# Optimization experiments

Hardware: AMD Instinct MI355X
Metric: run time of the kernel (lower is better)

The kernel has to match this reference:

```python
import jax, jax.numpy as jnp
import numpy as np

N_ATOMS, N_EDGES, N_TRIPLES = 5000, 200000, 4000000
D_NODE, D_EDGE, N_BASIS = 128, 128, 9


def setup_inputs() -> dict:
    key = jax.random.key(0)
    ks = jax.random.split(key, 14)
    inp = {
        "node_feat": jax.random.normal(ks[0], (N_ATOMS, D_NODE), jnp.float32),
        "edge_feat": jax.random.normal(ks[1], (N_EDGES, D_EDGE), jnp.float32),
        "three_basis": jax.random.normal(ks[2], (N_TRIPLES, N_BASIS), jnp.float32),
        "three_cutoff": jax.random.uniform(ks[3], (N_EDGES,), jnp.float32),
        # learned params: update_network_atom = Linear(d_node->n_basis) + sigmoid
        "W_atom": jax.random.normal(ks[4], (D_NODE, N_BASIS), jnp.float32) / np.sqrt(D_NODE).astype(np.float32),
        "b_atom": jnp.zeros((N_BASIS,), jnp.float32),
        # update_network_bond = gated MLP: silu(Linear) * sigmoid(Linear), n_basis->d_edge
        "W_gate": jax.random.normal(ks[5], (N_BASIS, D_EDGE), jnp.float32) / np.sqrt(N_BASIS).astype(np.float32),
        "b_gate": jnp.zeros((D_EDGE,), jnp.float32),
        "W_sig": jax.random.normal(ks[6], (N_BASIS, D_EDGE), jnp.float32) / np.sqrt(N_BASIS).astype(np.float32),
        "b_sig": jnp.zeros((D_EDGE,), jnp.float32),
        # graph structure (int constants)
        "graph_dst": jax.random.randint(ks[7], (N_EDGES,), 0, N_ATOMS, jnp.int32),
        "lg_src": jax.random.randint(ks[8], (N_TRIPLES,), 0, N_EDGES, jnp.int32),
        "lg_dst": jax.random.randint(ks[9], (N_TRIPLES,), 0, N_EDGES, jnp.int32),
        # sorted segment ids == get_segment_indices_from_n(n_triple_ij)
        "segment_ids": jnp.sort(jax.random.randint(ks[10], (N_TRIPLES,), 0, N_EDGES, jnp.int32)),
    }
    return inp


def reference(node_feat, edge_feat, three_basis, three_cutoff,
              W_atom, b_atom, W_gate, b_gate, W_sig, b_sig,
              graph_dst, lg_src, lg_dst, segment_ids):
    # Eq.2: transform node features, gather end atom of each triple's second bond
    atoms = jax.nn.sigmoid(node_feat @ W_atom + b_atom)          # [n_atoms, n_basis]
    end_atom_index = graph_dst[lg_dst]                           # [n_triples]
    basis = three_basis * atoms[end_atom_index]                  # [n_triples, n_basis]
    # cutoff weights per triple (dead code in the provided source: scatter uses basis)
    weights = three_cutoff[lg_src] * three_cutoff[lg_dst]        # [n_triples]
    _ = basis * weights[:, None]
    # scatter-sum triples back to their bond
    new_bonds = jax.ops.segment_sum(basis, segment_ids, num_segments=N_EDGES)  # [n_edges, n_basis]
    # Eq.3: gated MLP bond update
    update = jax.nn.silu(new_bonds @ W_gate + b_gate) * jax.nn.sigmoid(new_bonds @ W_sig + b_sig)
    return edge_feat + update
```

## Files before the change

kernel.cpp:

```cpp
#include <hip/hip_runtime.h>

#define D_NODE    128
#define N_BASIS   9
#define AH_STRIDE 16
#define D_EDGE    128

#define BLOCK_C 512
#define TPT     2
#define CHUNK   (BLOCK_C * TPT)
#define SEG_CAP 384

typedef _Float16 half8 __attribute__((ext_vector_type(8)));

#define AS1(p) ((const __attribute__((address_space(1))) void*)(p))
#define AS3(p) ((__attribute__((address_space(3))) void*)(p))

__device__ __forceinline__ float fast_sigmoid(float x) {
    return __builtin_amdgcn_rcpf(1.0f + __expf(-x));
}

__global__ __launch_bounds__(256) void atoms_kernel(
    const float* __restrict__ node_feat,
    const float* __restrict__ W_atom,
    const float* __restrict__ b_atom,
    _Float16* __restrict__ atoms, int n_atoms)
{
    __shared__ float sW[D_NODE * N_BASIS];
    for (int t = threadIdx.x; t < D_NODE * N_BASIS; t += 256)
        sW[t] = W_atom[t];
    __syncthreads();
    int idx = blockIdx.x * 256 + threadIdx.x;
    int total = n_atoms * N_BASIS;
    if (idx >= total) return;
    int a = idx / N_BASIS;
    int b = idx - a * N_BASIS;
    const float* row = node_feat + a * D_NODE;
    float acc = b_atom[b];
#pragma unroll 8
    for (int i = 0; i < D_NODE; ++i)
        acc += row[i] * sW[i * N_BASIS + b];
    atoms[a * AH_STRIDE + b] = (_Float16)fast_sigmoid(acc);
}

#define FLUSH_RUN()                                                          \
    do {                                                                     \
        if (use_lds) {                                                       \
            float* dst_ = lacc + (cur - seg_first) * N_BASIS;                \
            _Pragma("unroll")                                                \
            for (int k_ = 0; k_ < N_BASIS; ++k_)                             \
                atomicAdd(&dst_[k_], sum[k_]);                               \
        } else {                                                             \
            float* dst_ = new_bonds + (size_t)cur * N_BASIS;                 \
            _Pragma("unroll")                                                \
            for (int k_ = 0; k_ < N_BASIS; ++k_)                             \
                unsafeAtomicAdd(&dst_[k_], sum[k_]);                         \
        }                                                                    \
    } while (0)

__global__ __launch_bounds__(BLOCK_C) void triple_kernel(
    const float* __restrict__ three_basis,
    const _Float16* __restrict__ atoms,
    const int*   __restrict__ graph_dst,
    const int*   __restrict__ lg_dst,
    const int*   __restrict__ seg,
    float* __restrict__ new_bonds,
    int n_triples)
{
    __shared__ float stb[CHUNK * N_BASIS];
    __shared__ float lacc[SEG_CAP * N_BASIS];
    __shared__ int sh_first, sh_last;

    const int tid = threadIdx.x;
    const int chunk_start = blockIdx.x * CHUNK;
    const int t0 = chunk_start + tid * TPT;

    {
        int avail = (n_triples - chunk_start) * (N_BASIS * 4);
        int full_bytes = avail > CHUNK * N_BASIS * 4 ? CHUNK * N_BASIS * 4 : avail;
        int nfull = full_bytes >> 4;
        const char* gsrc = (const char*)three_basis + (size_t)chunk_start * (N_BASIS * 4);
        const int lane = tid & 63;
        for (int base = (tid >> 6) * 64; base < nfull; base += BLOCK_C) {
            int i = base + lane;
            if (i < nfull) {
                __builtin_amdgcn_global_load_lds(
                    AS1(gsrc + (size_t)i * 16),
                    AS3((char*)stb + (size_t)base * 16),
                    16, 0, 0);
            }
        }
        int rem = full_bytes - (nfull << 4);
        if ((tid << 2) < rem)
            ((float*)stb)[nfull * 4 + tid] = ((const float*)gsrc)[nfull * 4 + tid];
    }

    if (tid == 0) sh_first = seg[chunk_start];
    if (tid == BLOCK_C - 1) {
        int last = chunk_start + CHUNK;
        if (last > n_triples) last = n_triples;
        sh_last = seg[last - 1];
    }
    for (int i = tid; i < SEG_CAP * N_BASIS; i += BLOCK_C)
        lacc[i] = 0.0f;

    const bool fast = (t0 + TPT <= n_triples);
    int sg0 = 0, sg1 = 0;
    half8 h0, h1;
    _Float16 e0h = (_Float16)0.f, e1h = (_Float16)0.f;
    if (fast) {
        int2 sg2 = *(const int2*)(seg + t0);
        int2 ld2 = *(const int2*)(lg_dst + t0);
        sg0 = sg2.x; sg1 = sg2.y;
        int ai0 = graph_dst[ld2.x];
        int ai1 = graph_dst[ld2.y];
        const _Float16* ap0 = atoms + (size_t)ai0 * AH_STRIDE;
        const _Float16* ap1 = atoms + (size_t)ai1 * AH_STRIDE;
        h0 = *(const half8*)ap0;
        h1 = *(const half8*)ap1;
        e0h = ap0[8];
        e1h = ap1[8];
    }

    __syncthreads();

    const int seg_first = sh_first;
    const int range = sh_last - seg_first + 1;
    const bool use_lds = (range <= SEG_CAP);

    if (fast) {
        const float* tbl = stb + tid * (TPT * N_BASIS);
        float sum[N_BASIS];
        int cur = sg0;
#pragma unroll
        for (int k = 0; k < 8; ++k) sum[k] = tbl[k] * (float)h0[k];
        sum[8] = tbl[8] * (float)e0h;
        if (sg1 != cur) {
            FLUSH_RUN();
            cur = sg1;
#pragma unroll
            for (int k = 0; k < 8; ++k) sum[k] = tbl[N_BASIS + k] * (float)h1[k];
            sum[8] = tbl[N_BASIS + 8] * (float)e1h;
        } else {
#pragma unroll
            for (int k = 0; k < 8; ++k) sum[k] += tbl[N_BASIS + k] * (float)h1[k];
            sum[8] += tbl[N_BASIS + 8] * (float)e1h;
        }
        FLUSH_RUN();
    } else if (t0 < n_triples) {
        int tend = t0 + TPT; if (tend > n_triples) tend = n_triples;
        for (int t = t0; t < tend; ++t) {
            int cur = seg[t];
            int atom = graph_dst[lg_dst[t]];
            const float* tbr = three_basis + (size_t)t * N_BASIS;
            const _Float16* ar = atoms + (size_t)atom * AH_STRIDE;
            float sum[N_BASIS];
#pragma unroll
            for (int k = 0; k < N_BASIS; ++k) sum[k] = tbr[k] * (float)ar[k];
            FLUSH_RUN();
        }
    }

    __syncthreads();

    if (use_lds) {
        int total = range * N_BASIS;
        for (int idx = tid; idx < total; idx += BLOCK_C) {
            int r = idx / N_BASIS;
            int k = idx - r * N_BASIS;
            float v = lacc[idx];
            int s = seg_first + r;
            if (r == 0 || r == range - 1) {
                if (v != 0.0f)
                    unsafeAtomicAdd(&new_bonds[(size_t)s * N_BASIS + k], v);
            } else {
                new_bonds[(size_t)s * N_BASIS + k] = v;
            }
        }
    }
}

__global__ __launch_bounds__(256) void mlp_kernel(
    const float* __restrict__ edge_feat,
    const float* __restrict__ new_bonds,
    const float* __restrict__ W_gate, const float* __restrict__ b_gate,
    const float* __restrict__ W_sig,  const float* __restrict__ b_sig,
    float* __restrict__ out, int n_edges)
{
    const int tid  = threadIdx.x;
    const int grp  = tid >> 5;
    const int c    = (tid & 31) * 4;
    const int e0   = (blockIdx.x * 8 + grp) * 4;
    if (e0 >= n_edges) return;
    const int nvalid = (n_edges - e0) < 4 ? (n_edges - e0) : 4;

    float nb[4][N_BASIS];
#pragma unroll
    for (int j = 0; j < 4; ++j) {
        const float* nbr = new_bonds + (size_t)(e0 + (j < nvalid ? j : 0)) * N_BASIS;
#pragma unroll
        for (int k = 0; k < N_BASIS; ++k) nb[j][k] = nbr[k];
    }

    float4 bg = *(const float4*)(b_gate + c);
    float4 bs = *(const float4*)(b_sig + c);
    float4 g[4], s[4];
#pragma unroll
    for (int j = 0; j < 4; ++j) { g[j] = bg; s[j] = bs; }

#pragma unroll
    for (int k = 0; k < N_BASIS; ++k) {
        float4 wg = *(const float4*)(W_gate + k * D_EDGE + c);
        float4 ws = *(const float4*)(W_sig  + k * D_EDGE + c);
#pragma unroll
        for (int j = 0; j < 4; ++j) {
            g[j].x += nb[j][k] * wg.x; g[j].y += nb[j][k] * wg.y;
            g[j].z += nb[j][k] * wg.z; g[j].w += nb[j][k] * wg.w;
            s[j].x += nb[j][k] * ws.x; s[j].y += nb[j][k] * ws.y;
            s[j].z += nb[j][k] * ws.z; s[j].w += nb[j][k] * ws.w;
        }
    }

#pragma unroll
    for (int j = 0; j < 4; ++j) {
        if (j < nvalid) {
            int e = e0 + j;
            float4 ef = *(const float4*)(edge_feat + (size_t)e * D_EDGE + c);
            float4 o;
            o.x = ef.x + g[j].x * fast_sigmoid(g[j].x) * fast_sigmoid(s[j].x);
            o.y = ef.y + g[j].y * fast_sigmoid(g[j].y) * fast_sigmoid(s[j].y);
            o.z = ef.z + g[j].z * fast_sigmoid(g[j].z) * fast_sigmoid(s[j].z);
            o.w = ef.w + g[j].w * fast_sigmoid(g[j].w) * fast_sigmoid(s[j].w);
            *(float4*)(out + (size_t)e * D_EDGE + c) = o;
        }
    }
}

extern "C" void kernel_launch(void* const* d_in, const int* in_sizes, int n_in,
                              void* d_out, int out_size, void* d_ws, size_t ws_size,
                              hipStream_t stream) {
    const float* node_feat   = (const float*)d_in[0];
    const float* edge_feat   = (const float*)d_in[1];
    const float* three_basis = (const float*)d_in[2];
    const float* W_atom      = (const float*)d_in[4];
    const float* b_atom      = (const float*)d_in[5];
    const float* W_gate      = (const float*)d_in[6];
    const float* b_gate      = (const float*)d_in[7];
    const float* W_sig       = (const float*)d_in[8];
    const float* b_sig       = (const float*)d_in[9];
    const int*   graph_dst   = (const int*)d_in[10];
    const int*   lg_dst      = (const int*)d_in[12];
    const int*   seg         = (const int*)d_in[13];

    int n_atoms   = in_sizes[0] / D_NODE;
    int n_edges   = in_sizes[1] / D_EDGE;
    int n_triples = in_sizes[2] / N_BASIS;

    _Float16* atoms = (_Float16*)d_ws;
    size_t atoms_bytes = ((size_t)n_atoms * AH_STRIDE * sizeof(_Float16) + 255) & ~(size_t)255;
    float* new_bonds = (float*)((char*)d_ws + atoms_bytes);
    size_t nb_bytes = (size_t)n_edges * N_BASIS * sizeof(float);

    hipMemsetAsync(new_bonds, 0, nb_bytes, stream);

    atoms_kernel<<<(n_atoms * N_BASIS + 255) / 256, 256, 0, stream>>>(
        node_feat, W_atom, b_atom, atoms, n_atoms);

    triple_kernel<<<(n_triples + CHUNK - 1) / CHUNK, BLOCK_C, 0, stream>>>(
        three_basis, atoms, graph_dst, lg_dst, seg, new_bonds, n_triples);

    mlp_kernel<<<(n_edges + 31) / 32, 256, 0, stream>>>(
        edge_feat, new_bonds, W_gate, b_gate, W_sig, b_sig, (float*)d_out, n_edges);
}
```

Before: 474.8 us.

## Pre-gather per-edge atom rows and load triple basis directly into registers

Adds a kernel that precomputes an edge-indexed fp16 table of atom features, so each triple does one dependent gather instead of two (graph_dst then atoms). The triple kernel drops the global_load_lds staging of three_basis into LDS and reads each thread's 4 triples as 9 float4 loads into registers. The block shape changes from 512 threads × 2 triples to 256 × 4, and the LDS segment capacity rises to 512. The cost is an extra kernel launch and a 200k-row table that is larger and less cache-resident than the 5000-row atom table. The edge-table path is used only when the workspace is large enough.

```diff
diff --git a/kernel.cpp b/kernel.cpp
--- a/kernel.cpp
+++ b/kernel.cpp
@@ -5,15 +5,12 @@
 #define AH_STRIDE 16
 #define D_EDGE    128
 
-#define BLOCK_C 512
-#define TPT     2
+#define BLOCK_C 256
+#define TPT     4
 #define CHUNK   (BLOCK_C * TPT)
-#define SEG_CAP 384
+#define SEG_CAP 512
 
 typedef _Float16 half8 __attribute__((ext_vector_type(8)));
-
-#define AS1(p) ((const __attribute__((address_space(1))) void*)(p))
-#define AS3(p) ((__attribute__((address_space(3))) void*)(p))
 
 __device__ __forceinline__ float fast_sigmoid(float x) {
     return __builtin_amdgcn_rcpf(1.0f + __expf(-x));
@@ -42,6 +39,22 @@
     atoms[a * AH_STRIDE + b] = (_Float16)fast_sigmoid(acc);
 }
 
+__global__ __launch_bounds__(256) void edge_atoms_kernel(
+    const _Float16* __restrict__ atoms,
+    const int* __restrict__ graph_dst,
+    _Float16* __restrict__ ea, int n_edges)
+{
+    int e = blockIdx.x * 256 + threadIdx.x;
+    if (e >= n_edges) return;
+    int a = graph_dst[e];
+    const _Float16* ap = atoms + (size_t)a * AH_STRIDE;
+    half8 h = *(const half8*)ap;
+    _Float16 h8 = ap[8];
+    _Float16* dp = ea + (size_t)e * AH_STRIDE;
+    *(half8*)dp = h;
+    dp[8] = h8;
+}
+
 #define FLUSH_RUN()                                                          \
     do {                                                                     \
         if (use_lds) {                                                       \
@@ -57,42 +70,22 @@
         }                                                                    \
     } while (0)
 
+template<bool EA>
 __global__ __launch_bounds__(BLOCK_C) void triple_kernel(
     const float* __restrict__ three_basis,
-    const _Float16* __restrict__ atoms,
+    const _Float16* __restrict__ atab,
     const int*   __restrict__ graph_dst,
     const int*   __restrict__ lg_dst,
     const int*   __restrict__ seg,
     float* __restrict__ new_bonds,
     int n_triples)
 {
-    __shared__ float stb[CHUNK * N_BASIS];
     __shared__ float lacc[SEG_CAP * N_BASIS];
     __shared__ int sh_first, sh_last;
 
     const int tid = threadIdx.x;
     const int chunk_start = blockIdx.x * CHUNK;
     const int t0 = chunk_start + tid * TPT;
-
-    {
-        int avail = (n_triples - chunk_start) * (N_BASIS * 4);
-        int full_bytes = avail > CHUNK * N_BASIS * 4 ? CHUNK * N_BASIS * 4 : avail;
-        int nfull = full_bytes >> 4;
-        const char* gsrc = (const char*)three_basis + (size_t)chunk_start * (N_BASIS * 4);
-        const int lane = tid & 63;
-        for (int base = (tid >> 6) * 64; base < nfull; base += BLOCK_C) {
-            int i = base + lane;
-            if (i < nfull) {
-                __builtin_amdgcn_global_load_lds(
-                    AS1(gsrc + (size_t)i * 16),
-                    AS3((char*)stb + (size_t)base * 16),
-                    16, 0, 0);
-            }
-        }
-        int rem = full_bytes - (nfull << 4);
-        if ((tid << 2) < rem)
-            ((float*)stb)[nfull * 4 + tid] = ((const float*)gsrc)[nfull * 4 + tid];
-    }
 
     if (tid == 0) sh_first = seg[chunk_start];
     if (tid == BLOCK_C - 1) {
@@ -102,57 +95,66 @@
     }
     for (int i = tid; i < SEG_CAP * N_BASIS; i += BLOCK_C)
         lacc[i] = 0.0f;
-
-    const bool fast = (t0 + TPT <= n_triples);
-    int sg0 = 0, sg1 = 0;
-    half8 h0, h1;
-    _Float16 e0h = (_Float16)0.f, e1h = (_Float16)0.f;
-    if (fast) {
-        int2 sg2 = *(const int2*)(seg + t0);
-        int2 ld2 = *(const int2*)(lg_dst + t0);
-        sg0 = sg2.x; sg1 = sg2.y;
-        int ai0 = graph_dst[ld2.x];
-        int ai1 = graph_dst[ld2.y];
-        const _Float16* ap0 = atoms + (size_t)ai0 * AH_STRIDE;
-        const _Float16* ap1 = atoms + (size_t)ai1 * AH_STRIDE;
-        h0 = *(const half8*)ap0;
-        h1 = *(const half8*)ap1;
-        e0h = ap0[8];
-        e1h = ap1[8];
-    }
-
     __syncthreads();
 
     const int seg_first = sh_first;
     const int range = sh_last - seg_first + 1;
     const bool use_lds = (range <= SEG_CAP);
 
-    if (fast) {
-        const float* tbl = stb + tid * (TPT * N_BASIS);
+    if (t0 + TPT <= n_triples) {
+        float tb[TPT * N_BASIS];
+        const float4* tb4 = (const float4*)(three_basis + (size_t)t0 * N_BASIS);
+#pragma unroll
+        for (int q = 0; q < 9; ++q)
+            *(float4*)&tb[q * 4] = tb4[q];
+
+        const int4 sg4 = *(const int4*)(seg + t0);
+        const int4 ld4 = *(const int4*)(lg_dst + t0);
+        int sgs[TPT] = { sg4.x, sg4.y, sg4.z, sg4.w };
+
+        int ridx[TPT];
+        if (EA) {
+            ridx[0] = ld4.x; ridx[1] = ld4.y; ridx[2] = ld4.z; ridx[3] = ld4.w;
+        } else {
+            ridx[0] = graph_dst[ld4.x];
+            ridx[1] = graph_dst[ld4.y];
+            ridx[2] = graph_dst[ld4.z];
+            ridx[3] = graph_dst[ld4.w];
+        }
+        half8 hh[TPT];
+        _Float16 h8[TPT];
+#pragma unroll
+        for (int i = 0; i < TPT; ++i) {
+            const _Float16* ap = atab + (size_t)ridx[i] * AH_STRIDE;
+            hh[i] = *(const half8*)ap;
+            h8[i] = ap[8];
+        }
+
         float sum[N_BASIS];
-        int cur = sg0;
-#pragma unroll
-        for (int k = 0; k < 8; ++k) sum[k] = tbl[k] * (float)h0[k];
-        sum[8] = tbl[8] * (float)e0h;
-        if (sg1 != cur) {
-            FLUSH_RUN();
-            cur = sg1;
-#pragma unroll
-            for (int k = 0; k < 8; ++k) sum[k] = tbl[N_BASIS + k] * (float)h1[k];
-            sum[8] = tbl[N_BASIS + 8] * (float)e1h;
-        } else {
-#pragma unroll
-            for (int k = 0; k < 8; ++k) sum[k] += tbl[N_BASIS + k] * (float)h1[k];
-            sum[8] += tbl[N_BASIS + 8] * (float)e1h;
+        int cur = sgs[0];
+#pragma unroll
+        for (int k = 0; k < N_BASIS; ++k) sum[k] = 0.0f;
+
+#pragma unroll
+        for (int i = 0; i < TPT; ++i) {
+            if (sgs[i] != cur) {
+                FLUSH_RUN();
+                cur = sgs[i];
+#pragma unroll
+                for (int k = 0; k < N_BASIS; ++k) sum[k] = 0.0f;
+            }
+#pragma unroll
+            for (int k = 0; k < 8; ++k)
+                sum[k] += tb[i * N_BASIS + k] * (float)hh[i][k];
+            sum[8] += tb[i * N_BASIS + 8] * (float)h8[i];
         }
         FLUSH_RUN();
     } else if (t0 < n_triples) {
-        int tend = t0 + TPT; if (tend > n_triples) tend = n_triples;
-        for (int t = t0; t < tend; ++t) {
+        for (int t = t0; t < n_triples; ++t) {
             int cur = seg[t];
-            int atom = graph_dst[lg_dst[t]];
+            int r = EA ? lg_dst[t] : graph_dst[lg_dst[t]];
             const float* tbr = three_basis + (size_t)t * N_BASIS;
-            const _Float16* ar = atoms + (size_t)atom * AH_STRIDE;
+            const _Float16* ar = atab + (size_t)r * AH_STRIDE;
             float sum[N_BASIS];
 #pragma unroll
             for (int k = 0; k < N_BASIS; ++k) sum[k] = tbr[k] * (float)ar[k];
@@ -255,18 +257,30 @@
     int n_edges   = in_sizes[1] / D_EDGE;
     int n_triples = in_sizes[2] / N_BASIS;
 
+    size_t atoms_bytes = ((size_t)n_atoms * AH_STRIDE * sizeof(_Float16) + 255) & ~(size_t)255;
+    size_t ea_bytes    = ((size_t)n_edges * AH_STRIDE * sizeof(_Float16) + 255) & ~(size_t)255;
+    size_t nb_bytes    = (size_t)n_edges * N_BASIS * sizeof(float);
+
+    bool use_ea = (ws_size >= atoms_bytes + ea_bytes + nb_bytes);
+
     _Float16* atoms = (_Float16*)d_ws;
-    size_t atoms_bytes = ((size_t)n_atoms * AH_STRIDE * sizeof(_Float16) + 255) & ~(size_t)255;
-    float* new_bonds = (float*)((char*)d_ws + atoms_bytes);
-    size_t nb_bytes = (size_t)n_edges * N_BASIS * sizeof(float);
+    _Float16* ea    = (_Float16*)((char*)d_ws + atoms_bytes);
+    float* new_bonds = (float*)((char*)d_ws + atoms_bytes + (use_ea ? ea_bytes : 0));
 
     hipMemsetAsync(new_bonds, 0, nb_bytes, stream);
 
     atoms_kernel<<<(n_atoms * N_BASIS + 255) / 256, 256, 0, stream>>>(
         node_feat, W_atom, b_atom, atoms, n_atoms);
 
-    triple_kernel<<<(n_triples + CHUNK - 1) / CHUNK, BLOCK_C, 0, stream>>>(
-        three_basis, atoms, graph_dst, lg_dst, seg, new_bonds, n_triples);
+    if (use_ea) {
+        edge_atoms_kernel<<<(n_edges + 255) / 256, 256, 0, stream>>>(
+            atoms, graph_dst, ea, n_edges);
+        triple_kernel<true><<<(n_triples + CHUNK - 1) / CHUNK, BLOCK_C, 0, stream>>>(
+            three_basis, ea, graph_dst, lg_dst, seg, new_bonds, n_triples);
+    } else {
+        triple_kernel<false><<<(n_triples + CHUNK - 1) / CHUNK, BLOCK_C, 0, stream>>>(
+            three_basis, atoms, graph_dst, lg_dst, seg, new_bonds, n_triples);
+    }
 
     mlp_kernel<<<(n_edges + 31) / 32, 256, 0, stream>>>(
         edge_feat, new_bonds, W_gate, b_gate, W_sig, b_sig, (float*)d_out, n_edges);
```

Result: faster. 420.5 us (-11.5%).
